# Performance work log

Hardware: AMD Instinct MI355X
Metric: run time of the kernel (lower is better)

## Reference

```python
import jax, jax.numpy as jnp
import numpy as np

DIM = 1  # quantization axis (channels)


def setup_inputs() -> dict:
    key = jax.random.key(0)
    kx, kc = jax.random.split(key)
    x = jax.random.normal(kx, (32, 256, 32, 32), dtype=jnp.float32)
    # nn.init.normal_(weight, 0, 1.1)
    codebook = 1.1 * jax.random.normal(kc, (8192, 256), dtype=jnp.float32)
    return {"x": x, "codebook": codebook}


def reference(x, codebook):
    # move quantization dim to last: [B, C, H, W] -> [B, W, H, C]
    xt = jnp.swapaxes(x, -1, DIM)
    flat = xt.reshape(-1, xt.shape[-1])  # [N, D]
    # squared distances ||f - c||^2 = ||f||^2 - 2 f.c + ||c||^2  -> [N, K]
    d2 = (jnp.sum(flat * flat, axis=1, keepdims=True)
          - 2.0 * (flat @ codebook.T)
          + jnp.sum(codebook * codebook, axis=1))
    idx = jnp.argmin(d2, axis=1)                      # [N]
    codes = codebook[idx].reshape(xt.shape)           # nearest-code gather
    indices = idx.reshape(xt.shape[:-1])
    # transpose back to original layout
    codes = jnp.swapaxes(codes, -1, DIM)              # [B, C, H, W]
    indices = jnp.swapaxes(indices, -1, DIM)          # [B, H, W]
    return codes, indices
```

## Files before the change

kernel.cpp:

```cpp
#include <hip/hip_runtime.h>
#include <math.h>


typedef _Float16 v8h __attribute__((ext_vector_type(8)));
typedef float f32x16 __attribute__((ext_vector_type(16)));
typedef unsigned int u32;

#define MFMA16 __builtin_amdgcn_mfma_f32_32x32x16_f16

__device__ __forceinline__ void gll16(const _Float16* g, _Float16* l) {
  __builtin_amdgcn_global_load_lds(
      (const __attribute__((address_space(1))) void*)(const void*)g,
      (__attribute__((address_space(3))) void*)(void*)l, 16, 0, 0);
}

__global__ __launch_bounds__(256) void cnorm_k(const float4* __restrict__ cb4,
                                               float* __restrict__ cn) {
  int lane = threadIdx.x & 63;
  int row = (blockIdx.x << 2) + (threadIdx.x >> 6);
  float4 v = cb4[(size_t)row * 64 + lane];
  float s = v.x * v.x + v.y * v.y + v.z * v.z + v.w * v.w;
#pragma unroll
  for (int off = 32; off > 0; off >>= 1) s += __shfl_xor(s, off, 64);
  if (lane == 0) cn[row] = s;
}

__global__ __launch_bounds__(256) void split_cb(const float4* __restrict__ cb4,
                                                _Float16* __restrict__ W) {
  const int j = threadIdx.x & 31;
  const int ks = j >> 1, hi = j & 1;
  const int r = (blockIdx.x << 3) + (threadIdx.x >> 5);
  const float4* src = cb4 + (size_t)r * 64 + (ks << 2) + (hi << 1);
  float4 v0 = src[0], v1 = src[1];
  float t[8] = {v0.x, v0.y, v0.z, v0.w, v1.x, v1.y, v1.z, v1.w};
  v8h hv, mv;
#pragma unroll
  for (int i = 0; i < 8; ++i) {
    float vs = t[i] * 8192.f;
    _Float16 h = (_Float16)vs;
    _Float16 m = (_Float16)(vs - (float)h);
    hv[i] = h; mv[i] = m;
  }
  const int wv = (r >> 6) & 7, c64 = r & 63;
  _Float16* base = W + ((size_t)((r >> 9) << 4) + ks) * 16384 + (wv << 11);
  *(v8h*)(base + (hi << 9) + (c64 << 3)) = hv;
  *(v8h*)(base + 1024 + (hi << 9) + (c64 << 3)) = mv;
}

#define STEP_BODY(P, Q, DO_CNV)                                              \
  if (st < 254) {                                                            \
    const _Float16* gsrc = W + ((size_t)(st + 2) << 14) + chunk + (lane << 3); \
    gll16(gsrc,        &Bsh[P][chunk]);                                      \
    gll16(gsrc + 512,  &Bsh[P][chunk + 512]);                                \
    gll16(gsrc + 1024, &Bsh[P][chunk + 1024]);                               \
    gll16(gsrc + 1536, &Bsh[P][chunk + 1536]);                               \
    asm volatile("s_waitcnt vmcnt(4)" ::: "memory");                         \
  } else {                                                                   \
    asm volatile("s_waitcnt vmcnt(0)" ::: "memory");                         \
  }                                                                          \
  __builtin_amdgcn_sched_barrier(0);                                         \
  if (DO_CNV) {                 \
    cnv0 = cn[(ct << 9) + (w << 6) + col];                                   \
    cnv1 = cn[(ct << 9) + (w << 6) + 32 + col];                              \
  }                                                                          \
  if (st < 255) {                                                            \
    const int ko = (((st + 1) & 15) << 4) + (hi << 3);                       \
    Af[Q][0] = *(const v8h*)&F2[0][col][ko];                                 \
    Af[Q][1] = *(const v8h*)&F2[0][32 + col][ko];                            \
    Af[Q][2] = *(const v8h*)&F2[1][col][ko];                                 \
    Af[Q][3] = *(const v8h*)&F2[1][32 + col][ko];                            \
    const _Float16* Bb = &Bsh[Q][0];                                         \
    Bf[Q][0] = *(const v8h*)&Bb[rb0];                                        \
    Bf[Q][1] = *(const v8h*)&Bb[rb0 + 256];                                  \
    Bf[Q][2] = *(const v8h*)&Bb[rb0 + 1024];                                 \
    Bf[Q][3] = *(const v8h*)&Bb[rb0 + 1280];                                 \
  }                                                                          \
  __builtin_amdgcn_s_setprio(1);                                             \
  a00 = MFMA16(Af[P][0], Bf[P][0], a00, 0, 0, 0);                            \
  a01 = MFMA16(Af[P][0], Bf[P][1], a01, 0, 0, 0);                            \
  a10 = MFMA16(Af[P][1], Bf[P][0], a10, 0, 0, 0);                            \
  a11 = MFMA16(Af[P][1], Bf[P][1], a11, 0, 0, 0);                            \
  a00 = MFMA16(Af[P][0], Bf[P][2], a00, 0, 0, 0);                            \
  a01 = MFMA16(Af[P][0], Bf[P][3], a01, 0, 0, 0);                            \
  a10 = MFMA16(Af[P][1], Bf[P][2], a10, 0, 0, 0);                            \
  a11 = MFMA16(Af[P][1], Bf[P][3], a11, 0, 0, 0);                            \
  a00 = MFMA16(Af[P][2], Bf[P][0], a00, 0, 0, 0);                            \
  a01 = MFMA16(Af[P][2], Bf[P][1], a01, 0, 0, 0);                            \
  a10 = MFMA16(Af[P][3], Bf[P][0], a10, 0, 0, 0);                            \
  a11 = MFMA16(Af[P][3], Bf[P][1], a11, 0, 0, 0);                            \
  __builtin_amdgcn_s_setprio(0);                                             \
  asm volatile("s_waitcnt lgkmcnt(0)" ::: "memory");  \
  __builtin_amdgcn_sched_barrier(0);

__global__ void __launch_bounds__(512, 1) vq_fast(const float* __restrict__ x,
                                                  const float4* __restrict__ cb4,
                                                  const float* __restrict__ cn,
                                                  const _Float16* __restrict__ W,
                                                  float* __restrict__ out) {
  __shared__ __align__(16) _Float16 F2[2][64][264];
  __shared__ __align__(16) _Float16 Bsh[2][16384];
  __shared__ float fnP[64][8];
  __shared__ float fnS[64];
  __shared__ float wredS[8][64];
  __shared__ u32  wredC[8][64];
  __shared__ u32  finS[64];

  const int tid = threadIdx.x;
  const int lane = tid & 63;
  const int w = tid >> 6;
  const int col = lane & 31;
  const int hi = lane >> 5;
  const int b = blockIdx.x >> 4;
  const int h0 = (blockIdx.x & 15) << 1;

  const int chunk = w << 11;
  const int rb0 = chunk + (hi << 9) + (col << 3);

  {
    const _Float16* s0 = W + chunk + (lane << 3);
#pragma unroll
    for (int k = 0; k < 4; ++k) gll16(s0 + (k << 9), &Bsh[0][chunk + (k << 9)]);
#pragma unroll
    for (int k = 0; k < 4; ++k) gll16(s0 + 16384 + (k << 9), &Bsh[1][chunk + (k << 9)]);
  }

  {
    const float* xb = x + ((size_t)b << 18) + (h0 << 5);
    float s = 0.f;
#pragma unroll
    for (int j = 0; j < 4; ++j) {
      v8h hv, mv;
#pragma unroll
      for (int i = 0; i < 8; ++i) {
        const int c = (w << 5) + (j << 3) + i;
        float v = xb[(size_t)c * 1024 + lane];
        s += v * v;
        float vs = v * 8192.f;
        _Float16 h = (_Float16)vs;
        _Float16 m = (_Float16)(vs - (float)h);
        hv[i] = h; mv[i] = m;
      }
      *(v8h*)&F2[0][lane][(w << 5) + (j << 3)] = hv;
      *(v8h*)&F2[1][lane][(w << 5) + (j << 3)] = mv;
    }
    fnP[lane][w] = s;
  }
  __syncthreads();
  if (tid < 64) {
    float t = 0.f;
#pragma unroll
    for (int j = 0; j < 8; ++j) t += fnP[tid][j];
    fnS[tid] = t;
  }
  __syncthreads();

  float fnr[32];
#pragma unroll
  for (int sl = 0; sl < 32; ++sl) {
    const int row = ((sl >> 4) << 5) + (sl & 3) + (((sl >> 2) & 3) << 3) + (hi << 2);
    fnr[sl] = fnS[row];
  }

  v8h Af[2][4], Bf[2][4];
  {
    const int ko = (hi << 3);
    Af[0][0] = *(const v8h*)&F2[0][col][ko];
    Af[0][1] = *(const v8h*)&F2[0][32 + col][ko];
    Af[0][2] = *(const v8h*)&F2[1][col][ko];
    Af[0][3] = *(const v8h*)&F2[1][32 + col][ko];
    const _Float16* Bb = &Bsh[0][0];
    Bf[0][0] = *(const v8h*)&Bb[rb0];
    Bf[0][1] = *(const v8h*)&Bb[rb0 + 256];
    Bf[0][2] = *(const v8h*)&Bb[rb0 + 1024];
    Bf[0][3] = *(const v8h*)&Bb[rb0 + 1280];
  }
  asm volatile("s_waitcnt lgkmcnt(0)" ::: "memory");
  __builtin_amdgcn_sched_barrier(0);

  f32x16 a00, a01, a10, a11;
#pragma unroll
  for (int r = 0; r < 16; ++r) { a00[r] = 0.f; a01[r] = 0.f; a10[r] = 0.f; a11[r] = 0.f; }
  float mn[32];
#pragma unroll
  for (int sl = 0; sl < 32; ++sl) mn[sl] = INFINITY;
  u32 idp[8] = {0, 0, 0, 0, 0, 0, 0, 0};

#pragma unroll 1
  for (int ct = 0; ct < 16; ++ct) {
    float cnv0, cnv1;
#pragma unroll
    for (int kk = 0; kk < 8; ++kk) {
      {
        const int st = (ct << 4) + (kk << 1);
        STEP_BODY(0, 1, (kk == 0))
      }
      {
        const int st = (ct << 4) + (kk << 1) + 1;
        STEP_BODY(1, 0, false)
      }
    }
#pragma unroll
    for (int sl = 0; sl < 32; ++sl) {
      const int Mb = sl >> 4, reg = sl & 15;
      const float base = fnr[sl];
      const u32 sh = (u32)((sl & 3) << 3);
      {
        const float d = (Mb == 0) ? a00[reg] : a10[reg];
        float s = (base + (-0x1p-25f) * d) + cnv0;
        const bool better = s < mn[sl];
        const u32 curv = idp[sl >> 2];
        const u32 upd = (curv & ~(255u << sh)) | (((u32)(ct << 1)) << sh);
        idp[sl >> 2] = better ? upd : curv;
        mn[sl] = better ? s : mn[sl];
      }
      {
        const float d = (Mb == 0) ? a01[reg] : a11[reg];
        float s = (base + (-0x1p-25f) * d) + cnv1;
        const bool better = s < mn[sl];
        const u32 curv = idp[sl >> 2];
        const u32 upd = (curv & ~(255u << sh)) | (((u32)((ct << 1) | 1)) << sh);
        idp[sl >> 2] = better ? upd : curv;
        mn[sl] = better ? s : mn[sl];
      }
    }
#pragma unroll
    for (int r = 0; r < 16; ++r) { a00[r] = 0.f; a01[r] = 0.f; a10[r] = 0.f; a11[r] = 0.f; }
  }

#pragma unroll
  for (int sl = 0; sl < 32; ++sl) {
    float v = mn[sl];
    const u32 byte = (idp[sl >> 2] >> ((sl & 3) << 3)) & 255u;
    u32 code = ((byte >> 1) << 9) + ((u32)w << 6) + ((byte & 1) << 5) + (u32)col;
#pragma unroll
    for (int off = 1; off < 32; off <<= 1) {
      float v2 = __shfl_xor(v, off, 64);
      u32 c2 = (u32)__shfl_xor((int)code, off, 64);
      if (v2 < v || (v2 == v && c2 < code)) { v = v2; code = c2; }
    }
    if (col == 0) {
      const int row = ((sl >> 4) << 5) + (sl & 3) + (((sl >> 2) & 3) << 3) + (hi << 2);
      wredS[w][row] = v; wredC[w][row] = code;
    }
  }
  __syncthreads();
  if (tid < 64) {
    float bv = wredS[0][tid]; u32 bc = wredC[0][tid];
#pragma unroll
    for (int j = 1; j < 8; ++j) {
      float vv = wredS[j][tid]; u32 cc = wredC[j][tid];
      if (vv < bv || (vv == bv && cc < bc)) { bv = vv; bc = cc; }
    }
    finS[tid] = bc;
    out[(size_t)8388608 + ((size_t)b << 10) + (h0 << 5) + tid] = (float)bc;
  }
  __syncthreads();

  {
    const int pt = tid & 63, cg = tid >> 6;
    const u32 code = finS[pt];
    const float4* cbr = cb4 + ((size_t)code << 6);
    const size_t obase = ((size_t)b << 18) + (h0 << 5) + pt;
#pragma unroll
    for (int cc = 0; cc < 8; ++cc) {
      const int c4 = (cc << 3) + cg;
      float4 vv = cbr[c4];
      out[obase + (size_t)((c4 << 2) + 0) * 1024] = vv.x;
      out[obase + (size_t)((c4 << 2) + 1) * 1024] = vv.y;
      out[obase + (size_t)((c4 << 2) + 2) * 1024] = vv.z;
      out[obase + (size_t)((c4 << 2) + 3) * 1024] = vv.w;
    }
  }
}

__global__ void __launch_bounds__(512, 2) vq_fb(const float* __restrict__ x,
                                                const float4* __restrict__ cb4,
                                                const float* __restrict__ cn,
                                                float* __restrict__ out) {
  __shared__ __align__(16) _Float16 F2[2][64][264];
  __shared__ __align__(16) _Float16 Bsh[512][72];
  __shared__ float fnP[64][8];
  __shared__ float fnS[64];
  __shared__ float wredS[8][64];
  __shared__ u32  wredC[8][64];
  __shared__ u32  finS[64];

  const int tid = threadIdx.x;
  const int lane = tid & 63;
  const int w = tid >> 6;
  const int col = lane & 31;
  const int hi = lane >> 5;
  const int b = blockIdx.x >> 4;
  const int h0 = (blockIdx.x & 15) << 1;

  float4 rg[8];
  {
    const float4* src = cb4 + ((size_t)tid << 6);
#pragma unroll
    for (int j = 0; j < 8; ++j) rg[j] = src[j];
  }
  {
    const float* xb = x + ((size_t)b << 18) + (h0 << 5);
    float s = 0.f;
#pragma unroll
    for (int j = 0; j < 4; ++j) {
      v8h hv, mv;
#pragma unroll
      for (int i = 0; i < 8; ++i) {
        const int c = (w << 5) + (j << 3) + i;
        float v = xb[(size_t)c * 1024 + lane];
        s += v * v;
        float vs = v * 8192.f;
        _Float16 h = (_Float16)vs;
        _Float16 m = (_Float16)(vs - (float)h);
        hv[i] = h; mv[i] = m;
      }
      *(v8h*)&F2[0][lane][(w << 5) + (j << 3)] = hv;
      *(v8h*)&F2[1][lane][(w << 5) + (j << 3)] = mv;
    }
    fnP[lane][w] = s;
  }
  __syncthreads();
  if (tid < 64) {
    float t = 0.f;
#pragma unroll
    for (int j = 0; j < 8; ++j) t += fnP[tid][j];
    fnS[tid] = t;
  }
  {
#pragma unroll
    for (int j = 0; j < 4; ++j) {
      float t0[8] = {rg[2*j].x, rg[2*j].y, rg[2*j].z, rg[2*j].w,
                     rg[2*j+1].x, rg[2*j+1].y, rg[2*j+1].z, rg[2*j+1].w};
      v8h hv, mv;
#pragma unroll
      for (int i = 0; i < 8; ++i) {
        float vs = t0[i] * 8192.f;
        _Float16 h = (_Float16)vs;
        _Float16 m = (_Float16)(vs - (float)h);
        hv[i] = h; mv[i] = m;
      }
      *(v8h*)&Bsh[tid][(j << 3)] = hv;
      *(v8h*)&Bsh[tid][32 + (j << 3)] = mv;
    }
  }
  __syncthreads();

  float fnr[32];
#pragma unroll
  for (int sl = 0; sl < 32; ++sl) {
    const int row = ((sl >> 4) << 5) + (sl & 3) + (((sl >> 2) & 3) << 3) + (hi << 2);
    fnr[sl] = fnS[row];
  }

  f32x16 acc[2][2];
#pragma unroll
  for (int r = 0; r < 16; ++r) {
    acc[0][0][r] = 0.f; acc[0][1][r] = 0.f; acc[1][0][r] = 0.f; acc[1][1][r] = 0.f;
  }
  float mn[32];
#pragma unroll
  for (int sl = 0; sl < 32; ++sl) mn[sl] = INFINITY;
  u32 idp[8] = {0, 0, 0, 0, 0, 0, 0, 0};
  float cnv0 = 0.f, cnv1 = 0.f;

  for (int st = 0; st < 128; ++st) {
    const int ks = st & 7, ct = st >> 3;
    if (st < 127) {
      const int tn = st + 1;
      const float4* src = cb4 + ((size_t)((((tn >> 3) << 9) + tid)) << 6) + ((tn & 7) << 3);
#pragma unroll
      for (int j = 0; j < 8; ++j) rg[j] = src[j];
    }
    if (ks == 0) {
      cnv0 = cn[(ct << 9) + (w << 6) + col];
      cnv1 = cn[(ct << 9) + (w << 6) + 32 + col];
    }
    const int kb = ks << 5;
#pragma unroll
    for (int kh = 0; kh < 2; ++kh) {
      const int ko = kb + (kh << 4) + (hi << 3);
      const v8h ah0 = *(const v8h*)&F2[0][col][ko];
      const v8h ah1 = *(const v8h*)&F2[0][32 + col][ko];
      const v8h am0 = *(const v8h*)&F2[1][col][ko];
      const v8h am1 = *(const v8h*)&F2[1][32 + col][ko];
      const int bo = (kh << 4) + (hi << 3);
      const v8h bh0 = *(const v8h*)&Bsh[(w << 6) + col][bo];
      const v8h bh1 = *(const v8h*)&Bsh[(w << 6) + 32 + col][bo];
      const v8h bm0 = *(const v8h*)&Bsh[(w << 6) + col][32 + bo];
      const v8h bm1 = *(const v8h*)&Bsh[(w << 6) + 32 + col][32 + bo];
      acc[0][0] = MFMA16(ah0, bh0, acc[0][0], 0, 0, 0);
      acc[0][0] = MFMA16(ah0, bm0, acc[0][0], 0, 0, 0);
      acc[0][0] = MFMA16(am0, bh0, acc[0][0], 0, 0, 0);
      acc[0][1] = MFMA16(ah0, bh1, acc[0][1], 0, 0, 0);
      acc[0][1] = MFMA16(ah0, bm1, acc[0][1], 0, 0, 0);
      acc[0][1] = MFMA16(am0, bh1, acc[0][1], 0, 0, 0);
      acc[1][0] = MFMA16(ah1, bh0, acc[1][0], 0, 0, 0);
      acc[1][0] = MFMA16(ah1, bm0, acc[1][0], 0, 0, 0);
      acc[1][0] = MFMA16(am1, bh0, acc[1][0], 0, 0, 0);
      acc[1][1] = MFMA16(ah1, bh1, acc[1][1], 0, 0, 0);
      acc[1][1] = MFMA16(ah1, bm1, acc[1][1], 0, 0, 0);
      acc[1][1] = MFMA16(am1, bh1, acc[1][1], 0, 0, 0);
    }
    if (ks == 7) {
#pragma unroll
      for (int sl = 0; sl < 32; ++sl) {
        const int Mb = sl >> 4, reg = sl & 15;
        const float base = fnr[sl];
        const u32 sh = (u32)((sl & 3) << 3);
        {
          float s = (base + (-0x1p-25f) * acc[Mb][0][reg]) + cnv0;
          const bool better = s < mn[sl];
          const u32 curv = idp[sl >> 2];
          const u32 upd = (curv & ~(255u << sh)) | (((u32)(ct << 1)) << sh);
          idp[sl >> 2] = better ? upd : curv;
          mn[sl] = better ? s : mn[sl];
        }
        {
          float s = (base + (-0x1p-25f) * acc[Mb][1][reg]) + cnv1;
          const bool better = s < mn[sl];
          const u32 curv = idp[sl >> 2];
          const u32 upd = (curv & ~(255u << sh)) | (((u32)((ct << 1) | 1)) << sh);
          idp[sl >> 2] = better ? upd : curv;
          mn[sl] = better ? s : mn[sl];
        }
      }
#pragma unroll
      for (int r = 0; r < 16; ++r) {
        acc[0][0][r] = 0.f; acc[0][1][r] = 0.f; acc[1][0][r] = 0.f; acc[1][1][r] = 0.f;
      }
    }
    v8h cr[8];
    if (st < 127) {
#pragma unroll
      for (int j = 0; j < 4; ++j) {
        float t0[8] = {rg[2*j].x, rg[2*j].y, rg[2*j].z, rg[2*j].w,
                       rg[2*j+1].x, rg[2*j+1].y, rg[2*j+1].z, rg[2*j+1].w};
#pragma unroll
        for (int i = 0; i < 8; ++i) {
          float vs = t0[i] * 8192.f;
          _Float16 h = (_Float16)vs;
          _Float16 m = (_Float16)(vs - (float)h);
          cr[j][i] = h; cr[4 + j][i] = m;
        }
      }
    }
    __syncthreads();
    if (st < 127) {
#pragma unroll
      for (int j = 0; j < 4; ++j) {
        *(v8h*)&Bsh[tid][(j << 3)] = cr[j];
        *(v8h*)&Bsh[tid][32 + (j << 3)] = cr[4 + j];
      }
    }
    __syncthreads();
  }

#pragma unroll
  for (int sl = 0; sl < 32; ++sl) {
    float v = mn[sl];
    const u32 byte = (idp[sl >> 2] >> ((sl & 3) << 3)) & 255u;
    u32 code = ((byte >> 1) << 9) + ((u32)w << 6) + ((byte & 1) << 5) + (u32)col;
#pragma unroll
    for (int off = 1; off < 32; off <<= 1) {
      float v2 = __shfl_xor(v, off, 64);
      u32 c2 = (u32)__shfl_xor((int)code, off, 64);
      if (v2 < v || (v2 == v && c2 < code)) { v = v2; code = c2; }
    }
    if (col == 0) {
      const int row = ((sl >> 4) << 5) + (sl & 3) + (((sl >> 2) & 3) << 3) + (hi << 2);
      wredS[w][row] = v; wredC[w][row] = code;
    }
  }
  __syncthreads();
  if (tid < 64) {
    float bv = wredS[0][tid]; u32 bc = wredC[0][tid];
#pragma unroll
    for (int j = 1; j < 8; ++j) {
      float vv = wredS[j][tid]; u32 cc = wredC[j][tid];
      if (vv < bv || (vv == bv && cc < bc)) { bv = vv; bc = cc; }
    }
    finS[tid] = bc;
    out[(size_t)8388608 + ((size_t)b << 10) + (h0 << 5) + tid] = (float)bc;
  }
  __syncthreads();
  {
    const int pt = tid & 63, cg = tid >> 6;
    const u32 code = finS[pt];
    const float4* cbr = cb4 + ((size_t)code << 6);
    const size_t obase = ((size_t)b << 18) + (h0 << 5) + pt;
#pragma unroll
    for (int cc = 0; cc < 8; ++cc) {
      const int c4 = (cc << 3) + cg;
      float4 vv = cbr[c4];
      out[obase + (size_t)((c4 << 2) + 0) * 1024] = vv.x;
      out[obase + (size_t)((c4 << 2) + 1) * 1024] = vv.y;
      out[obase + (size_t)((c4 << 2) + 2) * 1024] = vv.z;
      out[obase + (size_t)((c4 << 2) + 3) * 1024] = vv.w;
    }
  }
}

extern "C" void kernel_launch(void* const* d_in, const int* in_sizes, int n_in,
                              void* d_out, int out_size, void* d_ws, size_t ws_size,
                              hipStream_t stream) {
  const float* x = (const float*)d_in[0];
  const float* cb = (const float*)d_in[1];
  float* out = (float*)d_out;
  float* cnorm = (float*)d_ws;

  cnorm_k<<<2048, 256, 0, stream>>>((const float4*)cb, cnorm);
  if (ws_size >= (size_t)32768 + (size_t)8388608) {
    _Float16* W = (_Float16*)((char*)d_ws + 32768);
    split_cb<<<1024, 256, 0, stream>>>((const float4*)cb, W);
    vq_fast<<<512, 512, 0, stream>>>(x, (const float4*)cb, cnorm, W, out);
  } else {
    vq_fb<<<512, 512, 0, stream>>>(x, (const float4*)cb, cnorm, out);
  }
}
```

Before: 465.8 us.

## Repack feature tile into MFMA-fragment LDS layout and relax step scheduling barriers

Replaces the padded row-major feature tile in LDS with a layout indexed by k-step, hi/lo split, row block, half and column, so each A-fragment read is a contiguous 16-byte load without bank conflicts and without padding. The step macro now waits on LDS reads at the start of the step instead of the end, hoists the codebook-norm load, and removes the sched_barriers and setprio hints. This lets the compiler interleave work more freely, at the risk of losing the hand-enforced MFMA/load ordering.

```diff
diff --git a/kernel.cpp b/kernel.cpp
--- a/kernel.cpp
+++ b/kernel.cpp
@@ -48,34 +48,33 @@
 }
 
 #define STEP_BODY(P, Q, DO_CNV)                                              \
+  asm volatile("s_waitcnt lgkmcnt(0)" ::: "memory");  \
+  if (DO_CNV) {             \
+    cnv0 = cn[(ct << 9) + (w << 6) + col];                                   \
+    cnv1 = cn[(ct << 9) + (w << 6) + 32 + col];                              \
+  }                                                                          \
   if (st < 254) {                                                            \
     const _Float16* gsrc = W + ((size_t)(st + 2) << 14) + chunk + (lane << 3); \
     gll16(gsrc,        &Bsh[P][chunk]);                                      \
     gll16(gsrc + 512,  &Bsh[P][chunk + 512]);                                \
     gll16(gsrc + 1024, &Bsh[P][chunk + 1024]);                               \
     gll16(gsrc + 1536, &Bsh[P][chunk + 1536]);                               \
-    asm volatile("s_waitcnt vmcnt(4)" ::: "memory");                         \
+    asm volatile("s_waitcnt vmcnt(4)" ::: "memory");  \
   } else {                                                                   \
     asm volatile("s_waitcnt vmcnt(0)" ::: "memory");                         \
   }                                                                          \
-  __builtin_amdgcn_sched_barrier(0);                                         \
-  if (DO_CNV) {                 \
-    cnv0 = cn[(ct << 9) + (w << 6) + col];                                   \
-    cnv1 = cn[(ct << 9) + (w << 6) + 32 + col];                              \
-  }                                                                          \
   if (st < 255) {                                                            \
-    const int ko = (((st + 1) & 15) << 4) + (hi << 3);                       \
-    Af[Q][0] = *(const v8h*)&F2[0][col][ko];                                 \
-    Af[Q][1] = *(const v8h*)&F2[0][32 + col][ko];                            \
-    Af[Q][2] = *(const v8h*)&F2[1][col][ko];                                 \
-    Af[Q][3] = *(const v8h*)&F2[1][32 + col][ko];                            \
+    const int ksq = (st + 1) & 15;                                           \
+    Af[Q][0] = *(const v8h*)&F2L[ksq][0][0][hi][col][0];                     \
+    Af[Q][1] = *(const v8h*)&F2L[ksq][0][1][hi][col][0];                     \
+    Af[Q][2] = *(const v8h*)&F2L[ksq][1][0][hi][col][0];                     \
+    Af[Q][3] = *(const v8h*)&F2L[ksq][1][1][hi][col][0];                     \
     const _Float16* Bb = &Bsh[Q][0];                                         \
     Bf[Q][0] = *(const v8h*)&Bb[rb0];                                        \
     Bf[Q][1] = *(const v8h*)&Bb[rb0 + 256];                                  \
     Bf[Q][2] = *(const v8h*)&Bb[rb0 + 1024];                                 \
     Bf[Q][3] = *(const v8h*)&Bb[rb0 + 1280];                                 \
   }                                                                          \
-  __builtin_amdgcn_s_setprio(1);                                             \
   a00 = MFMA16(Af[P][0], Bf[P][0], a00, 0, 0, 0);                            \
   a01 = MFMA16(Af[P][0], Bf[P][1], a01, 0, 0, 0);                            \
   a10 = MFMA16(Af[P][1], Bf[P][0], a10, 0, 0, 0);                            \
@@ -87,17 +86,14 @@
   a00 = MFMA16(Af[P][2], Bf[P][0], a00, 0, 0, 0);                            \
   a01 = MFMA16(Af[P][2], Bf[P][1], a01, 0, 0, 0);                            \
   a10 = MFMA16(Af[P][3], Bf[P][0], a10, 0, 0, 0);                            \
-  a11 = MFMA16(Af[P][3], Bf[P][1], a11, 0, 0, 0);                            \
-  __builtin_amdgcn_s_setprio(0);                                             \
-  asm volatile("s_waitcnt lgkmcnt(0)" ::: "memory");  \
-  __builtin_amdgcn_sched_barrier(0);
+  a11 = MFMA16(Af[P][3], Bf[P][1], a11, 0, 0, 0);
 
 __global__ void __launch_bounds__(512, 1) vq_fast(const float* __restrict__ x,
                                                   const float4* __restrict__ cb4,
                                                   const float* __restrict__ cn,
                                                   const _Float16* __restrict__ W,
                                                   float* __restrict__ out) {
-  __shared__ __align__(16) _Float16 F2[2][64][264];
+  __shared__ __align__(16) _Float16 F2L[16][2][2][2][32][8];
   __shared__ __align__(16) _Float16 Bsh[2][16384];
   __shared__ float fnP[64][8];
   __shared__ float fnS[64];
@@ -126,22 +122,27 @@
 
   {
     const float* xb = x + ((size_t)b << 18) + (h0 << 5);
+    const int Mb = lane >> 5, cl = lane & 31;
     float s = 0.f;
 #pragma unroll
-    for (int j = 0; j < 4; ++j) {
-      v8h hv, mv;
-#pragma unroll
-      for (int i = 0; i < 8; ++i) {
-        const int c = (w << 5) + (j << 3) + i;
-        float v = xb[(size_t)c * 1024 + lane];
-        s += v * v;
-        float vs = v * 8192.f;
-        _Float16 h = (_Float16)vs;
-        _Float16 m = (_Float16)(vs - (float)h);
-        hv[i] = h; mv[i] = m;
-      }
-      *(v8h*)&F2[0][lane][(w << 5) + (j << 3)] = hv;
-      *(v8h*)&F2[1][lane][(w << 5) + (j << 3)] = mv;
+    for (int j = 0; j < 2; ++j) {
+      const int ks = (w << 1) + j;
+#pragma unroll
+      for (int fh = 0; fh < 2; ++fh) {
+        v8h hv, mv;
+#pragma unroll
+        for (int i = 0; i < 8; ++i) {
+          const int c = (ks << 4) + (fh << 3) + i;
+          float v = xb[(size_t)c * 1024 + lane];
+          s += v * v;
+          float vs = v * 8192.f;
+          _Float16 h = (_Float16)vs;
+          _Float16 m = (_Float16)(vs - (float)h);
+          hv[i] = h; mv[i] = m;
+        }
+        *(v8h*)&F2L[ks][0][Mb][fh][cl][0] = hv;
+        *(v8h*)&F2L[ks][1][Mb][fh][cl][0] = mv;
+      }
     }
     fnP[lane][w] = s;
   }
@@ -163,19 +164,16 @@
 
   v8h Af[2][4], Bf[2][4];
   {
-    const int ko = (hi << 3);
-    Af[0][0] = *(const v8h*)&F2[0][col][ko];
-    Af[0][1] = *(const v8h*)&F2[0][32 + col][ko];
-    Af[0][2] = *(const v8h*)&F2[1][col][ko];
-    Af[0][3] = *(const v8h*)&F2[1][32 + col][ko];
+    Af[0][0] = *(const v8h*)&F2L[0][0][0][hi][col][0];
+    Af[0][1] = *(const v8h*)&F2L[0][0][1][hi][col][0];
+    Af[0][2] = *(const v8h*)&F2L[0][1][0][hi][col][0];
+    Af[0][3] = *(const v8h*)&F2L[0][1][1][hi][col][0];
     const _Float16* Bb = &Bsh[0][0];
     Bf[0][0] = *(const v8h*)&Bb[rb0];
     Bf[0][1] = *(const v8h*)&Bb[rb0 + 256];
     Bf[0][2] = *(const v8h*)&Bb[rb0 + 1024];
     Bf[0][3] = *(const v8h*)&Bb[rb0 + 1280];
   }
-  asm volatile("s_waitcnt lgkmcnt(0)" ::: "memory");
-  __builtin_amdgcn_sched_barrier(0);
 
   f32x16 a00, a01, a10, a11;
 #pragma unroll
```

New measurement: 449.1 us. 1.04x faster.
